# Optimization experiments

Hardware: AMD Instinct MI355X
Metric: run time of the kernel (lower is better)

The kernel has to match this reference:

```python
import jax, jax.numpy as jnp
import numpy as np

MAX_REL = 7  # maxRelativeDist

def _rel_pos_table(L, max_rel):
    # |i-j|, with distances beyond max_rel mapped to max_rel + log2(d - max_rel), clipped to [0, 2*max_rel]
    idx = jnp.arange(L)
    d = jnp.abs(idx[:, None] - idx[None, :]).astype(jnp.float32)
    far = d > max_rel
    d = jnp.where(far, max_rel + jnp.log2(jnp.maximum(d - max_rel, 1.0)), d)
    return jnp.clip(d, 0, 2 * max_rel).astype(jnp.int32)  # [L, L]

def setup_inputs() -> dict:
    key = jax.random.key(0)
    ks = jax.random.split(key, 16)
    B, L, C, P, H, DK = 8, 2048, 512, 64, 8, 64
    s = 0.02
    inp = {
        'qx': jax.random.normal(ks[0], (B, L, C), jnp.float32),
        'kx': jax.random.normal(ks[1], (B, L, C), jnp.float32),
        'vx': jax.random.normal(ks[2], (B, L, C), jnp.float32),
        'maskPAD': jnp.ones((B, L, L), jnp.int32),
        # pseudoAttn: Linear(C, P)
        'Wp': jax.random.normal(ks[3], (C, P), jnp.float32) * s,
        'bp': jnp.zeros((P,), jnp.float32),
        # WQ/WK: Linear(C, dkEnhance*DK*H) with dkEnhance=1
        'Wq': jax.random.normal(ks[4], (C, H * DK), jnp.float32) * s,
        'bq': jnp.zeros((H * DK,), jnp.float32),
        'Wk': jax.random.normal(ks[5], (C, H * DK), jnp.float32) * s,
        'bk': jnp.zeros((H * DK,), jnp.float32),
        'Wv': jax.random.normal(ks[6], (C, H * DK), jnp.float32) * s,
        'bv': jnp.zeros((H * DK,), jnp.float32),
        'Wo': jax.random.normal(ks[7], (H * DK, C), jnp.float32) * s,
        'bo': jnp.zeros((C,), jnp.float32),
        # relative position embeddings: [2*MAX_REL+1, H]
        'embK': jax.random.normal(ks[8], (2 * MAX_REL + 1, H), jnp.float32) * s,
        'embB': jax.random.normal(ks[9], (2 * MAX_REL + 1, H), jnp.float32) * s,
    }
    return inp

def reference(qx, kx, vx, maskPAD, Wp, bp, Wq, bq, Wk, bk, Wv, bv, Wo, bo, embK, embB):
    # dropout is identity (eval mode); preScores=None
    B, L, C = qx.shape
    H = embK.shape[1]
    DK = Wv.shape[1] // H
    P = Wp.shape[1]

    # pseudo-token compression
    pScore = vx @ Wp + bp                                   # [B, L, P]
    mask = (maskPAD[:, 0] == 0)[:, :, None]                 # [B, L, 1]
    pScore = jnp.where(mask, jnp.float32(-2.0 ** 15), pScore)
    pAlpha = jax.nn.softmax(pScore, axis=1)                 # softmax over L
    kxc = jnp.einsum('blp,blc->bpc', pAlpha, kx)            # [B, P, C]
    vxc = jnp.einsum('blp,blc->bpc', pAlpha, vx)            # [B, P, C]
    pAlpha_d = jax.lax.stop_gradient(pAlpha)

    # multi-head projections
    q = (qx @ Wq + bq).reshape(B, L, H, DK)                 # [B, L, H, DK]
    k = (kxc @ Wk + bk).reshape(B, P, H, DK)
    v = (vxc @ Wv + bv).reshape(B, P, H, DK)

    scores = jnp.einsum('blhd,bphd->bhlp', q, k) / np.sqrt(DK)  # [B, H, L, P]

    # relative-position modulation
    relTab = _rel_pos_table(L, MAX_REL)                     # [L, L] int
    Kmat = jnp.transpose(embK[relTab], (2, 1, 0))           # [H, L, L]
    Bmat = jnp.transpose(embB[relTab], (2, 1, 0))           # [H, L, L]
    Kterm = jnp.einsum('hlm,bmp->bhlp', Kmat, pAlpha_d)
    Bterm = jnp.einsum('hlm,bmp->bhlp', Bmat, pAlpha_d)
    scores = scores * Kterm + Bterm

    alpha = jax.nn.softmax(scores, axis=3)                  # over pseudo tokens
    z = jnp.einsum('bhlp,bphd->blhd', alpha, v).reshape(B, L, H * DK)
    z = z @ Wo + bo                                         # [B, L, C]
    return z, pScore, scores
```

## Files before the change

kernel.cpp:

```cpp
#include <hip/hip_runtime.h>


typedef __attribute__((ext_vector_type(8))) short bhalf8;
typedef __attribute__((ext_vector_type(4))) float fx4;

__device__ __forceinline__ unsigned short f2bf(float f) {
  union { float f; unsigned u; } v; v.f = f;
  unsigned u = v.u + 0x7fffu + ((v.u >> 16) & 1u);
  return (unsigned short)(u >> 16);
}
__device__ __forceinline__ float bf2f(unsigned short h) {
  union { unsigned u; float f; } v; v.u = ((unsigned)h) << 16;
  return v.f;
}
__device__ __forceinline__ void gld16(const void* g, void* l) {
  __builtin_amdgcn_global_load_lds(
      (const __attribute__((address_space(1))) void*)g,
      (__attribute__((address_space(3))) void*)l, 16, 0, 0);
}

template <int BM, int BN, int CMODE, int AF32, int KSPLIT>
__global__ __launch_bounds__(256)
void gemm_mfma(const void* __restrict__ Av, const unsigned short* __restrict__ BT,
               const float* __restrict__ bias, void* __restrict__ Cout,
               int K, int lda, int ldbt, int ldc, int HDIV,
               long sAb, long sAh, long sBb, long sBh, long sCb, long sCh, long sCk,
               const int* __restrict__ mpad, float* __restrict__ aux)
{
  constexpr int NA = BM / 16, NB = BN / 16, NT = NA + NB;
  constexpr int WM = BM / 2, WN = BN / 2, FM = WM / 16, FN = WN / 16;
  __shared__ __align__(16) unsigned short lds[NT * 512];
  const int t = threadIdx.x, l = t & 63, w = t >> 6;
  const int wr = w >> 1, wc = w & 1;
  const int zz = blockIdx.z, b = zz / HDIV, h = zz % HDIV;
  const int row0 = KSPLIT ? 0 : blockIdx.y * BM;
  const int koff = KSPLIT ? blockIdx.y * K : 0;
  const long cko = KSPLIT ? (long)blockIdx.y * sCk : 0;
  const int col0 = blockIdx.x * BN;
  const unsigned short* Ag = (const unsigned short*)Av + b * sAb + h * sAh + (long)row0 * lda + koff;
  const float* AgF = (const float*)Av + b * sAb + h * sAh + (long)row0 * lda + koff;
  const unsigned short* Bg = BT + b * sBb + h * sBh + (long)col0 * ldbt + koff;
  const int lr = l & 15, lc = l >> 4;

  fx4 acc[FM][FN];
#pragma unroll
  for (int i = 0; i < FM; ++i)
#pragma unroll
    for (int j = 0; j < FN; ++j) acc[i][j] = fx4{0.f, 0.f, 0.f, 0.f};

  for (int k0 = 0; k0 < K; k0 += 32) {
#pragma unroll
    for (int i = 0; i < NT / 4; ++i) {
      const int tile = w + i * 4;
      if constexpr (AF32 == 1) {
        if (tile < NA) {
          const float* gf = AgF + (long)(tile * 16 + lr) * lda + k0 + lc * 8;
          float4 x = *(const float4*)gf, y = *(const float4*)(gf + 4);
          bhalf8 pk;
          pk[0] = (short)f2bf(x.x); pk[1] = (short)f2bf(x.y);
          pk[2] = (short)f2bf(x.z); pk[3] = (short)f2bf(x.w);
          pk[4] = (short)f2bf(y.x); pk[5] = (short)f2bf(y.y);
          pk[6] = (short)f2bf(y.z); pk[7] = (short)f2bf(y.w);
          *(bhalf8*)&lds[tile * 512 + l * 8] = pk;
        } else {
          gld16(Bg + (long)((tile - NA) * 16 + lr) * ldbt + k0 + lc * 8, &lds[tile * 512]);
        }
      } else if constexpr (AF32 == 2) {
        if (tile < NA) {
          const float* gf = (const float*)Av + (long)zz * sAb + (long)blockIdx.y * 131072
                            + (long)(tile * 16 + lr) * 512 + k0 + lc * 8;
          float4 x = make_float4(0.f, 0.f, 0.f, 0.f), y = x;
#pragma unroll
          for (int c = 0; c < 4; ++c) {
            float4 a = *(const float4*)(gf + (long)c * 32768);
            float4 bq = *(const float4*)(gf + (long)c * 32768 + 4);
            x.x += a.x; x.y += a.y; x.z += a.z; x.w += a.w;
            y.x += bq.x; y.y += bq.y; y.z += bq.z; y.w += bq.w;
          }
          bhalf8 pk;
          pk[0] = (short)f2bf(x.x); pk[1] = (short)f2bf(x.y);
          pk[2] = (short)f2bf(x.z); pk[3] = (short)f2bf(x.w);
          pk[4] = (short)f2bf(y.x); pk[5] = (short)f2bf(y.y);
          pk[6] = (short)f2bf(y.z); pk[7] = (short)f2bf(y.w);
          *(bhalf8*)&lds[tile * 512 + l * 8] = pk;
        } else {
          gld16(Bg + (long)((tile - NA) * 16 + lr) * ldbt + k0 + lc * 8, &lds[tile * 512]);
        }
      } else {
        const unsigned short* g = (tile < NA)
            ? Ag + (long)(tile * 16 + lr) * lda + k0 + lc * 8
            : Bg + (long)((tile - NA) * 16 + lr) * ldbt + k0 + lc * 8;
        gld16(g, &lds[tile * 512]);
      }
    }
    __syncthreads();
    bhalf8 af[FM], bf[FN];
#pragma unroll
    for (int i = 0; i < FM; ++i) af[i] = *(const bhalf8*)&lds[(wr * FM + i) * 512 + l * 8];
#pragma unroll
    for (int j = 0; j < FN; ++j) bf[j] = *(const bhalf8*)&lds[(NA + wc * FN + j) * 512 + l * 8];
#pragma unroll
    for (int i = 0; i < FM; ++i)
#pragma unroll
      for (int j = 0; j < FN; ++j)
        acc[i][j] = __builtin_amdgcn_mfma_f32_16x16x32_bf16(af[i], bf[j], acc[i][j], 0, 0, 0);
    __syncthreads();
  }

  if constexpr (CMODE == 3) {
    __shared__ float tbuf[64][65];
#pragma unroll
    for (int fm = 0; fm < FM; ++fm) {
#pragma unroll
      for (int fn = 0; fn < FN; ++fn) {
        const int rg0 = row0 + wr * WM + fm * 16 + lc * 4;
        const int cg = col0 + wc * WN + fn * 16 + lr;
        const float bb = bias[cg];
#pragma unroll
        for (int jj = 0; jj < 4; ++jj) {
          const int rg = rg0 + jj;
          float vv = acc[fm][fn][jj] + bb;
          if (mpad[((long)(rg >> 11)) * (2048L * 2048) + (rg & 2047)] == 0) vv = -32768.f;
          __builtin_nontemporal_store(vv, (float*)Cout + (long)rg * ldc + cg);
          tbuf[rg - row0][cg] = vv;
        }
      }
    }
    __syncthreads();
    const int b0 = row0 >> 11, l0b = row0 & 2047;
    const int pp = t >> 2, li0 = (t & 3) * 16;
    float* dst = aux + ((long)b0 * 64 + pp) * 2048 + l0b + li0;
#pragma unroll
    for (int i = 0; i < 16; i += 4) {
      float4 o = make_float4(tbuf[li0 + i][pp],     tbuf[li0 + i + 1][pp],
                             tbuf[li0 + i + 2][pp], tbuf[li0 + i + 3][pp]);
      *(float4*)(dst + i) = o;
    }
  } else {
#pragma unroll
    for (int fm = 0; fm < FM; ++fm) {
#pragma unroll
      for (int fn = 0; fn < FN; ++fn) {
        const int rg0 = row0 + wr * WM + fm * 16 + lc * 4;
        const int cg = col0 + wc * WN + fn * 16 + lr;
        float bb = 0.f;
        if constexpr (CMODE == 4) {
          bb = (zz == 0) ? bias[cg] : ((const float*)mpad)[cg];
        } else {
          bb = bias ? bias[cg] : 0.f;
        }
#pragma unroll
        for (int jj = 0; jj < 4; ++jj) {
          const int rg = rg0 + jj;
          const float v = acc[fm][fn][jj] + bb;
          if constexpr (CMODE == 0) {
            ((float*)Cout)[b * sCb + h * sCh + cko + (long)rg * ldc + cg] = v;
          } else if constexpr (CMODE == 1) {
            ((unsigned short*)Cout)[b * sCb + h * sCh + (long)rg * ldc + cg] = f2bf(v);
          } else if constexpr (CMODE == 2) {
            ((unsigned short*)Cout)[(((long)(rg >> 6) * 8 + (cg >> 6)) * 64 + (cg & 63)) * 64 + (rg & 63)] = f2bf(v);
          } else if constexpr (CMODE == 4) {
            if (zz == 0)
              ((unsigned short*)Cout)[(long)rg * ldc + cg] = f2bf(v);
            else
              ((unsigned short*)Cout)[262144 + (((long)(rg >> 6) * 8 + (cg >> 6)) * 64 + (cg & 63)) * 64 + (rg & 63)] = f2bf(v);
          } else {
            __builtin_nontemporal_store(v, (float*)Cout + b * sCb + h * sCh + cko + (long)rg * ldc + cg);
          }
        }
      }
    }
  }
}

__device__ __forceinline__ void tr_body(float (*tile)[65], const float* __restrict__ in,
                                        unsigned short* __restrict__ out,
                                        int R, int Cd, int r0, int c0, int t)
{
  const int tr = t >> 4, tc4 = (t & 15) * 4;
#pragma unroll
  for (int pass = 0; pass < 4; ++pass) {
    int r = pass * 16 + tr;
    float4 v = *(const float4*)(in + (long)(r0 + r) * Cd + c0 + tc4);
    tile[r][tc4] = v.x; tile[r][tc4 + 1] = v.y; tile[r][tc4 + 2] = v.z; tile[r][tc4 + 3] = v.w;
  }
  __syncthreads();
#pragma unroll
  for (int pass = 0; pass < 4; ++pass) {
    int c = pass * 16 + tr;
    ushort4 o;
    o.x = f2bf(tile[tc4][c]);     o.y = f2bf(tile[tc4 + 1][c]);
    o.z = f2bf(tile[tc4 + 2][c]); o.w = f2bf(tile[tc4 + 3][c]);
    *(ushort4*)(out + (long)(c0 + c) * R + r0 + tc4) = o;
  }
}

__global__ __launch_bounds__(256)
void tconv_prep(const float* Wq, const float* Wk, const float* Wv, const float* Wo, const float* Wp,
                const float* kx, const float* vx,
                unsigned short* WqT, unsigned short* WkT, unsigned short* WvT,
                unsigned short* WoT, unsigned short* WpT,
                unsigned short* kxT, unsigned short* vxT)
{
  __shared__ float tile[64][65];
  const int z = blockIdx.z;
  const long LC = 2048L * 512;
  const float* in; unsigned short* out; int R, Cd;
  if (z < 5) {
    if (blockIdx.y >= 8) return;
    R = 512;
    switch (z) {
      case 0: in = Wq; out = WqT; Cd = 512; break;
      case 1: in = Wk; out = WkT; Cd = 512; break;
      case 2: in = Wv; out = WvT; Cd = 512; break;
      case 3: in = Wo; out = WoT; Cd = 512; break;
      default: in = Wp; out = WpT; Cd = 64; break;
    }
    if ((int)blockIdx.x * 64 >= Cd) return;
  } else {
    const int zz = z - 5;
    in = (zz < 8) ? kx + zz * LC : vx + (zz - 8) * LC;
    out = (zz < 8) ? kxT + zz * LC : vxT + (zz - 8) * LC;
    R = 2048; Cd = 512;
  }
  tr_body(tile, in, out, R, Cd, blockIdx.y * 64, blockIdx.x * 64, threadIdx.x);
}

__global__ __launch_bounds__(256)
void softmax_scan(const float* __restrict__ pScoreT,
                  unsigned short* __restrict__ PSb, unsigned short* __restrict__ pA_bf)
{
  __shared__ float red[256];
  const int p = blockIdx.x, b = blockIdx.y, t = threadIdx.x;
  const float* row = pScoreT + ((size_t)b * 64 + p) * 2048;
  float4 va = ((const float4*)row)[t * 2], vb = ((const float4*)row)[t * 2 + 1];
  float v[8] = {va.x, va.y, va.z, va.w, vb.x, vb.y, vb.z, vb.w};
  float mx = v[0];
#pragma unroll
  for (int i = 1; i < 8; ++i) mx = fmaxf(mx, v[i]);
  red[t] = mx; __syncthreads();
  for (int s = 128; s > 0; s >>= 1) { if (t < s) red[t] = fmaxf(red[t], red[t + s]); __syncthreads(); }
  float m = red[0]; __syncthreads();
  float e[8]; float s = 0.f;
#pragma unroll
  for (int i = 0; i < 8; ++i) { e[i] = expf(v[i] - m); s += e[i]; }
  red[t] = s; __syncthreads();
  for (int o = 1; o < 256; o <<= 1) {
    float x = (t >= o) ? red[t - o] : 0.f;
    __syncthreads(); red[t] += x; __syncthreads();
  }
  float inv = 1.0f / red[255];
  float run = red[t] - s;
  size_t base = ((size_t)b * 64 + p) * 2048 + (size_t)t * 8;
#pragma unroll
  for (int i = 0; i < 8; ++i) {
    run += e[i];
    PSb[base + i] = f2bf(run * inv);
    pA_bf[base + i] = f2bf(e[i] * inv);
  }
}

__global__ __launch_bounds__(256)
void kb_make2(const unsigned short* __restrict__ PSb,
              const float* __restrict__ embK, const float* __restrict__ embB,
              ushort2* __restrict__ KB)
{
  const int L = 2048, STR = 338;
  __shared__ unsigned short psw[64 * STR];
  __shared__ float eKs[16][8], eBs[16][8];
  const int t = threadIdx.x, b = blockIdx.y, l0 = blockIdx.x * 64;
  if (t < 128) {
    int r = t >> 3, h = t & 7;
    eKs[r][h] = (r < 15) ? embK[r * 8 + h] : 0.f;
    eBs[r][h] = (r < 15) ? embB[r * 8 + h] : 0.f;
  }
  const int W0 = l0 - 136;
  const int w = t >> 6, ln = t & 63;
  for (int pr = w * 16; pr < w * 16 + 16; ++pr) {
    const unsigned short* src = PSb + ((long)b * 64 + pr) * 2048;
#pragma unroll
    for (int pass = 0; pass < 6; ++pass) {
      int j = pass * 64 + ln;
      if (j < 337) {
        int g = (j == 336) ? (L - 1) : (W0 + j);
        g = g < 0 ? 0 : (g > L - 1 ? L - 1 : g);
        psw[pr * STR + j] = src[g];
      }
    }
  }
  __syncthreads();
  const int p = ln;
  const int Btab[14] = {0,1,2,3,4,5,6,8,10,14,22,38,70,134};
  for (int step = 0; step < 16; ++step) {
    const int l = l0 + w * 16 + step;
    float U[15];
#pragma unroll
    for (int r = 0; r < 14; ++r) {
      int hi = l + Btab[r]; hi = hi > L - 1 ? L - 1 : hi;
      float u = bf2f(psw[p * STR + (hi - W0)]);
      const int lo = l - 1 - Btab[r];
      if (lo >= 0) u -= bf2f(psw[p * STR + (lo - W0)]);
      U[r] = u;
    }
    U[14] = bf2f(psw[p * STR + 336]);
    for (int h = 0; h < 8; ++h) {
      float Kt = 0.f, Bt = 0.f;
#pragma unroll
      for (int r = 0; r < 15; ++r) {
        Kt = fmaf(eKs[r][h] - eKs[r + 1][h], U[r], Kt);
        Bt = fmaf(eBs[r][h] - eBs[r + 1][h], U[r], Bt);
      }
      ushort2 o; o.x = f2bf(Kt); o.y = f2bf(Bt);
      KB[(((long)(b * 8 + h)) * L + l) * 64 + p] = o;
    }
  }
}

__global__ __launch_bounds__(256)
void attn_fused(const unsigned short* __restrict__ qb,
                const unsigned short* __restrict__ kp,
                const unsigned short* __restrict__ vpT,
                const ushort2* __restrict__ KB,
                float* __restrict__ sc_out,
                unsigned short* __restrict__ zpre)
{
  const int L = 2048;
  __shared__ __align__(16) unsigned short stg[24 * 512];
  unsigned short* qkb = &stg[8 * 512];
  const int t = threadIdx.x, l = t & 63, w = t >> 6, lr = l & 15, lc = l >> 4;
  const int flat = blockIdx.y * 16 + blockIdx.x;
  const int swz = (flat & 7) * 128 + (flat >> 3);
  const int z = swz >> 4, b = z >> 3, h = z & 7;
  const int l0 = (swz & 15) * 128;
  const unsigned short* Ag = qb + ((long)(b * L + l0)) * 512 + h * 64;
  const unsigned short* Bg = kp + (long)b * 64 * 512 + h * 64;
#pragma unroll
  for (int i = 0; i < 6; ++i) {
    const int tile = w + i * 4;
    const unsigned short* g;
    if (tile < 16) { int rt = tile >> 1, ks = tile & 1; g = Ag + (long)(rt * 16 + lr) * 512 + ks * 32 + lc * 8; }
    else { int j = tile - 16; int rt = j >> 1, ks = j & 1; g = Bg + (long)(rt * 16 + lr) * 512 + ks * 32 + lc * 8; }
    gld16(g, &stg[tile * 512]);
  }
  __syncthreads();
  const int wr = w >> 1, wc = w & 1;
  fx4 acc[4][2];
#pragma unroll
  for (int i = 0; i < 4; ++i)
#pragma unroll
    for (int j = 0; j < 2; ++j) acc[i][j] = fx4{0.f, 0.f, 0.f, 0.f};
#pragma unroll
  for (int ks = 0; ks < 2; ++ks) {
    bhalf8 af[4], bf[2];
#pragma unroll
    for (int i = 0; i < 4; ++i) af[i] = *(const bhalf8*)&stg[((wr * 4 + i) * 2 + ks) * 512 + l * 8];
#pragma unroll
    for (int j = 0; j < 2; ++j) bf[j] = *(const bhalf8*)&stg[(16 + (wc * 2 + j) * 2 + ks) * 512 + l * 8];
#pragma unroll
    for (int i = 0; i < 4; ++i)
#pragma unroll
      for (int j = 0; j < 2; ++j)
        acc[i][j] = __builtin_amdgcn_mfma_f32_16x16x32_bf16(af[i], bf[j], acc[i][j], 0, 0, 0);
  }
  __syncthreads();
#pragma unroll
  for (int fm = 0; fm < 4; ++fm)
#pragma unroll
    for (int fn = 0; fn < 2; ++fn)
#pragma unroll
      for (int jj = 0; jj < 4; ++jj) {
        const int row = wr * 64 + fm * 16 + lc * 4 + jj;
        const int col = wc * 32 + fn * 16 + lr;
        *(unsigned short*)((char*)qkb + ((row * 128 + col * 2) ^ ((row & 7) << 4))) = f2bf(acc[fm][fn][jj]);
      }
  __syncthreads();
  {
    const unsigned short* Vg = vpT + ((long)(b * 8 + h)) * 64 * 64;
#pragma unroll
    for (int i = 0; i < 2; ++i) {
      const int tile = w + i * 4, rt = tile >> 1, ks = tile & 1;
      gld16(Vg + (long)(rt * 16 + lr) * 64 + ks * 32 + lc * 8, &stg[tile * 512]);
    }
  }
  const int p = l;
  const ushort2* kbb = KB + (((long)(b * 8 + h)) * L + l0) * 64 + p;
  float* scb = sc_out + ((long)(b * 8 + h) * L + l0) * 64 + p;
  for (int c = 0; c < 8; ++c) {
    const int rbase = w * 32 + c * 4;
    float sv[4];
#pragma unroll
    for (int il = 0; il < 4; ++il) {
      const int row = rbase + il;
      const ushort2 kb = kbb[(long)row * 64];
      const float qkv = bf2f(*(const unsigned short*)((const char*)qkb + ((row * 128 + p * 2) ^ ((row & 7) << 4))));
      sv[il] = qkv * 0.125f * bf2f(kb.x) + bf2f(kb.y);
      __builtin_nontemporal_store(sv[il], scb + (long)row * 64);
    }
    float mx[4] = {sv[0], sv[1], sv[2], sv[3]};
#pragma unroll
    for (int o = 32; o > 0; o >>= 1)
#pragma unroll
      for (int il = 0; il < 4; ++il) mx[il] = fmaxf(mx[il], __shfl_xor(mx[il], o, 64));
    float ex[4], sm[4];
#pragma unroll
    for (int il = 0; il < 4; ++il) { ex[il] = __expf(sv[il] - mx[il]); sm[il] = ex[il]; }
#pragma unroll
    for (int o = 32; o > 0; o >>= 1)
#pragma unroll
      for (int il = 0; il < 4; ++il) sm[il] += __shfl_xor(sm[il], o, 64);
#pragma unroll
    for (int il = 0; il < 4; ++il) {
      const int row = rbase + il;
      *(unsigned short*)((char*)qkb + ((row * 128 + p * 2) ^ ((row & 7) << 4))) = f2bf(ex[il] / sm[il]);
    }
  }
  __syncthreads();
  fx4 a2[4][2];
#pragma unroll
  for (int i = 0; i < 4; ++i)
#pragma unroll
    for (int j = 0; j < 2; ++j) a2[i][j] = fx4{0.f, 0.f, 0.f, 0.f};
#pragma unroll
  for (int ks = 0; ks < 2; ++ks) {
    bhalf8 paf[4], pvf[2];
#pragma unroll
    for (int i = 0; i < 4; ++i) {
      const int row = (wr * 4 + i) * 16 + lr;
      paf[i] = *(const bhalf8*)((const char*)qkb + ((row * 128 + ks * 64 + lc * 16) ^ ((row & 7) << 4)));
    }
#pragma unroll
    for (int j = 0; j < 2; ++j)
      pvf[j] = *(const bhalf8*)&stg[(((wc * 2 + j) * 2 + ks) * 512) + l * 8];
#pragma unroll
    for (int i = 0; i < 4; ++i)
#pragma unroll
      for (int j = 0; j < 2; ++j)
        a2[i][j] = __builtin_amdgcn_mfma_f32_16x16x32_bf16(paf[i], pvf[j], a2[i][j], 0, 0, 0);
  }
#pragma unroll
  for (int fm = 0; fm < 4; ++fm)
#pragma unroll
    for (int fn = 0; fn < 2; ++fn)
#pragma unroll
      for (int jj = 0; jj < 4; ++jj) {
        const int row = wr * 64 + fm * 16 + lc * 4 + jj;
        const int col = wc * 32 + fn * 16 + lr;
        zpre[((long)(b * L + l0 + row)) * 512 + h * 64 + col] = f2bf(a2[fm][fn][jj]);
      }
}

extern "C" void kernel_launch(void* const* d_in, const int* in_sizes, int n_in,
                              void* d_out, int out_size, void* d_ws, size_t ws_size,
                              hipStream_t stream)
{
  const int B = 8, L = 2048, C = 512, P = 64;
  const float* qx = (const float*)d_in[0];
  const float* kx = (const float*)d_in[1];
  const float* vx = (const float*)d_in[2];
  const int* maskPAD = (const int*)d_in[3];
  const float* Wp = (const float*)d_in[4];
  const float* bp = (const float*)d_in[5];
  const float* Wq = (const float*)d_in[6];
  const float* bq = (const float*)d_in[7];
  const float* Wk = (const float*)d_in[8];
  const float* bk = (const float*)d_in[9];
  const float* Wv = (const float*)d_in[10];
  const float* bv = (const float*)d_in[11];
  const float* Wo = (const float*)d_in[12];
  const float* bo = (const float*)d_in[13];
  const float* embK = (const float*)d_in[14];
  const float* embB = (const float*)d_in[15];

  float* z_out  = (float*)d_out;
  float* ps_out = z_out + (size_t)B * L * C;
  float* sc_out = ps_out + (size_t)B * L * P;

  char* w8 = (char*)d_ws;
  size_t o = 0;
  auto take = [&](size_t n) { char* r = w8 + o; o += n; return r; };
  unsigned short* R_A  = (unsigned short*)take(16777216);
  unsigned short* R_B  = (unsigned short*)take(16777216);
  unsigned short* kxT  = (unsigned short*)take(16777216);
  unsigned short* vxT  = (unsigned short*)take(16777216);
  unsigned short* WqT  = (unsigned short*)take(524288);
  unsigned short* WkT  = (unsigned short*)take(524288);
  unsigned short* WvT  = (unsigned short*)take(524288);
  unsigned short* WoT  = (unsigned short*)take(524288);
  unsigned short* WpT  = (unsigned short*)take(65536);
  float* pScoreT       = (float*)take(4194304);
  unsigned short* PSb  = (unsigned short*)take(2097152);
  unsigned short* pAbf = (unsigned short*)take(2097152);
  float* pbuf          = (float*)take(8388608);
  unsigned short* kp   = (unsigned short*)take(1048576);
  unsigned short* vpT  = kp + 262144;
  ushort2* KB          = (ushort2*)take(33554432);

  tconv_prep<<<dim3(8, 32, 21), 256, 0, stream>>>(
      Wq, Wk, Wv, Wo, Wp, kx, vx, WqT, WkT, WvT, WoT, WpT, kxT, vxT);
  gemm_mfma<64, 64, 3, 1, 0><<<dim3(1, 256, 1), 256, 0, stream>>>(
      vx, WpT, bp, ps_out, 512, 512, 512, 64, 1, 0, 0, 0, 0, 0, 0, 0, maskPAD, pScoreT);
  softmax_scan<<<dim3(P, B), 256, 0, stream>>>(pScoreT, PSb, pAbf);
  kb_make2<<<dim3(L / 64, B), 256, 0, stream>>>(PSb, embK, embB, KB);
  gemm_mfma<64, 128, 0, 0, 1><<<dim3(4, 4, 16), 256, 0, stream>>>(
      pAbf, kxT, nullptr, pbuf, 512, 2048, 2048, 512, 2,
      131072, 0, 1048576, 8388608, 131072, 1048576, 32768, nullptr, nullptr);
  gemm_mfma<64, 128, 4, 2, 0><<<dim3(4, 8, 2), 256, 0, stream>>>(
      pbuf, WkT, bk, kp, 512, 512, 512, 512, 1,
      1048576, 0, 262144, 0, 0, 0, 0, (const int*)bv, nullptr);
  gemm_mfma<128, 128, 1, 1, 0><<<dim3(4, 128, 1), 256, 0, stream>>>(
      qx, WqT, bq, R_B, 512, 512, 512, 512, 1, 0, 0, 0, 0, 0, 0, 0, nullptr, nullptr);
  attn_fused<<<dim3(16, 64), 256, 0, stream>>>(
      R_B, kp, vpT, KB, sc_out, R_A);
  gemm_mfma<128, 128, 5, 0, 0><<<dim3(4, 128, 1), 256, 0, stream>>>(
      R_A, WoT, bo, z_out, 512, 512, 512, 512, 1, 0, 0, 0, 0, 0, 0, 0, nullptr, nullptr);
}
```

Before: 221.4 us.

## Merge independent small kernels into combined launches and prefetch KB into registers

Measured after the change: 201.5 us. 9.0% less time.

```diff
diff --git a/kernel.cpp b/kernel.cpp
--- a/kernel.cpp
+++ b/kernel.cpp
@@ -20,23 +20,24 @@
 }
 
 template <int BM, int BN, int CMODE, int AF32, int KSPLIT>
-__global__ __launch_bounds__(256)
-void gemm_mfma(const void* __restrict__ Av, const unsigned short* __restrict__ BT,
-               const float* __restrict__ bias, void* __restrict__ Cout,
-               int K, int lda, int ldbt, int ldc, int HDIV,
-               long sAb, long sAh, long sBb, long sBh, long sCb, long sCh, long sCk,
-               const int* __restrict__ mpad, float* __restrict__ aux)
+__device__ __forceinline__ void gemm_body(
+    int bxx, int byy, int bzz, char* smemc,
+    const void* __restrict__ Av, const unsigned short* __restrict__ BT,
+    const float* __restrict__ bias, void* __restrict__ Cout,
+    int K, int lda, int ldbt, int ldc, int HDIV,
+    long sAb, long sAh, long sBb, long sBh, long sCb, long sCh, long sCk,
+    const int* __restrict__ mpad, float* __restrict__ aux)
 {
   constexpr int NA = BM / 16, NB = BN / 16, NT = NA + NB;
   constexpr int WM = BM / 2, WN = BN / 2, FM = WM / 16, FN = WN / 16;
-  __shared__ __align__(16) unsigned short lds[NT * 512];
+  unsigned short* lds = (unsigned short*)smemc;
   const int t = threadIdx.x, l = t & 63, w = t >> 6;
   const int wr = w >> 1, wc = w & 1;
-  const int zz = blockIdx.z, b = zz / HDIV, h = zz % HDIV;
-  const int row0 = KSPLIT ? 0 : blockIdx.y * BM;
-  const int koff = KSPLIT ? blockIdx.y * K : 0;
-  const long cko = KSPLIT ? (long)blockIdx.y * sCk : 0;
-  const int col0 = blockIdx.x * BN;
+  const int zz = bzz, b = zz / HDIV, h = zz % HDIV;
+  const int row0 = KSPLIT ? 0 : byy * BM;
+  const int koff = KSPLIT ? byy * K : 0;
+  const long cko = KSPLIT ? (long)byy * sCk : 0;
+  const int col0 = bxx * BN;
   const unsigned short* Ag = (const unsigned short*)Av + b * sAb + h * sAh + (long)row0 * lda + koff;
   const float* AgF = (const float*)Av + b * sAb + h * sAh + (long)row0 * lda + koff;
   const unsigned short* Bg = BT + b * sBb + h * sBh + (long)col0 * ldbt + koff;
@@ -67,7 +68,7 @@
         }
       } else if constexpr (AF32 == 2) {
         if (tile < NA) {
-          const float* gf = (const float*)Av + (long)zz * sAb + (long)blockIdx.y * 131072
+          const float* gf = (const float*)Av + (long)zz * sAb + (long)byy * 131072
                             + (long)(tile * 16 + lr) * 512 + k0 + lc * 8;
           float4 x = make_float4(0.f, 0.f, 0.f, 0.f), y = x;
 #pragma unroll
@@ -108,7 +109,7 @@
   }
 
   if constexpr (CMODE == 3) {
-    __shared__ float tbuf[64][65];
+    float (*tbuf)[65] = (float(*)[65])(smemc + NT * 1024);
 #pragma unroll
     for (int fm = 0; fm < FM; ++fm) {
 #pragma unroll
@@ -173,6 +174,118 @@
   }
 }
 
+template <int BM, int BN, int CMODE, int AF32, int KSPLIT>
+__global__ __launch_bounds__(256)
+void gemm_mfma(const void* __restrict__ Av, const unsigned short* __restrict__ BT,
+               const float* __restrict__ bias, void* __restrict__ Cout,
+               int K, int lda, int ldbt, int ldc, int HDIV,
+               long sAb, long sAh, long sBb, long sBh, long sCb, long sCh, long sCk,
+               const int* __restrict__ mpad, float* __restrict__ aux)
+{
+  constexpr int SM = (BM / 16 + BN / 16) * 1024 + (CMODE == 3 ? 16640 : 0);
+  __shared__ __align__(16) char smem[SM];
+  gemm_body<BM, BN, CMODE, AF32, KSPLIT>(blockIdx.x, blockIdx.y, blockIdx.z, smem,
+      Av, BT, bias, Cout, K, lda, ldbt, ldc, HDIV,
+      sAb, sAh, sBb, sBh, sCb, sCh, sCk, mpad, aux);
+}
+
+__device__ __forceinline__ void kb_body(int bx, int by, char* smemc,
+    const unsigned short* __restrict__ PSb,
+    const float* __restrict__ embK, const float* __restrict__ embB,
+    ushort2* __restrict__ KB)
+{
+  const int L = 2048, STR = 338;
+  unsigned short* psw = (unsigned short*)smemc;
+  float (*eKs)[8] = (float(*)[8])(smemc + 43264);
+  float (*eBs)[8] = (float(*)[8])(smemc + 43264 + 512);
+  const int t = threadIdx.x, b = by, l0 = bx * 64;
+  if (t < 128) {
+    int r = t >> 3, h = t & 7;
+    eKs[r][h] = (r < 15) ? embK[r * 8 + h] : 0.f;
+    eBs[r][h] = (r < 15) ? embB[r * 8 + h] : 0.f;
+  }
+  const int W0 = l0 - 136;
+  const int w = t >> 6, ln = t & 63;
+  for (int pr = w * 16; pr < w * 16 + 16; ++pr) {
+    const unsigned short* src = PSb + ((long)b * 64 + pr) * 2048;
+#pragma unroll
+    for (int pass = 0; pass < 6; ++pass) {
+      int j = pass * 64 + ln;
+      if (j < 337) {
+        int g = (j == 336) ? (L - 1) : (W0 + j);
+        g = g < 0 ? 0 : (g > L - 1 ? L - 1 : g);
+        psw[pr * STR + j] = src[g];
+      }
+    }
+  }
+  __syncthreads();
+  const int p = ln;
+  const int Btab[14] = {0,1,2,3,4,5,6,8,10,14,22,38,70,134};
+  for (int step = 0; step < 16; ++step) {
+    const int l = l0 + w * 16 + step;
+    float U[15];
+#pragma unroll
+    for (int r = 0; r < 14; ++r) {
+      int hi = l + Btab[r]; hi = hi > L - 1 ? L - 1 : hi;
+      float u = bf2f(psw[p * STR + (hi - W0)]);
+      const int lo = l - 1 - Btab[r];
+      if (lo >= 0) u -= bf2f(psw[p * STR + (lo - W0)]);
+      U[r] = u;
+    }
+    U[14] = bf2f(psw[p * STR + 336]);
+    for (int h = 0; h < 8; ++h) {
+      float Kt = 0.f, Bt = 0.f;
+#pragma unroll
+      for (int r = 0; r < 15; ++r) {
+        Kt = fmaf(eKs[r][h] - eKs[r + 1][h], U[r], Kt);
+        Bt = fmaf(eBs[r][h] - eBs[r + 1][h], U[r], Bt);
+      }
+      ushort2 o; o.x = f2bf(Kt); o.y = f2bf(Bt);
+      KB[(((long)(b * 8 + h)) * L + l) * 64 + p] = o;
+    }
+  }
+}
+
+__global__ __launch_bounds__(256)
+void combo1(const unsigned short* __restrict__ pAbf, const unsigned short* __restrict__ kxT,
+            float* __restrict__ pbuf,
+            const unsigned short* __restrict__ PSb,
+            const float* __restrict__ embK, const float* __restrict__ embB,
+            ushort2* __restrict__ KB)
+{
+  __shared__ __align__(16) char smem[44544];
+  const int id = blockIdx.x;
+  if (id < 256) {
+    gemm_body<64, 128, 0, 0, 1>(id & 3, (id >> 2) & 3, id >> 4, smem,
+        pAbf, kxT, nullptr, pbuf, 512, 2048, 2048, 512, 2,
+        131072, 0, 1048576, 8388608, 131072, 1048576, 32768, nullptr, nullptr);
+  } else {
+    const int r = id - 256;
+    kb_body(r & 31, r >> 5, smem, PSb, embK, embB, KB);
+  }
+}
+
+__global__ __launch_bounds__(256)
+void combo2(const float* __restrict__ pbuf, const unsigned short* __restrict__ WkT,
+            const float* __restrict__ bk, const float* __restrict__ bv,
+            unsigned short* __restrict__ kp,
+            const float* __restrict__ qx, const unsigned short* __restrict__ WqT,
+            const float* __restrict__ bq, unsigned short* __restrict__ qbf)
+{
+  __shared__ __align__(16) char smem[16384];
+  const int id = blockIdx.x;
+  if (id < 64) {
+    gemm_body<64, 128, 4, 2, 0>(id & 3, (id >> 2) & 7, id >> 5, smem,
+        pbuf, WkT, bk, kp, 512, 512, 512, 512, 1,
+        1048576, 0, 262144, 0, 0, 0, 0, (const int*)bv, nullptr);
+  } else {
+    const int r = id - 64;
+    gemm_body<128, 128, 1, 1, 0>(r & 3, r >> 2, 0, smem,
+        qx, WqT, bq, qbf, 512, 512, 512, 512, 1,
+        0, 0, 0, 0, 0, 0, 0, nullptr, nullptr);
+  }
+}
+
 __device__ __forceinline__ void tr_body(float (*tile)[65], const float* __restrict__ in,
                                         unsigned short* __restrict__ out,
                                         int R, int Cd, int r0, int c0, int t)
@@ -261,62 +374,6 @@
 }
 
 __global__ __launch_bounds__(256)
-void kb_make2(const unsigned short* __restrict__ PSb,
-              const float* __restrict__ embK, const float* __restrict__ embB,
-              ushort2* __restrict__ KB)
-{
-  const int L = 2048, STR = 338;
-  __shared__ unsigned short psw[64 * STR];
-  __shared__ float eKs[16][8], eBs[16][8];
-  const int t = threadIdx.x, b = blockIdx.y, l0 = blockIdx.x * 64;
-  if (t < 128) {
-    int r = t >> 3, h = t & 7;
-    eKs[r][h] = (r < 15) ? embK[r * 8 + h] : 0.f;
-    eBs[r][h] = (r < 15) ? embB[r * 8 + h] : 0.f;
-  }
-  const int W0 = l0 - 136;
-  const int w = t >> 6, ln = t & 63;
-  for (int pr = w * 16; pr < w * 16 + 16; ++pr) {
-    const unsigned short* src = PSb + ((long)b * 64 + pr) * 2048;
-#pragma unroll
-    for (int pass = 0; pass < 6; ++pass) {
-      int j = pass * 64 + ln;
-      if (j < 337) {
-        int g = (j == 336) ? (L - 1) : (W0 + j);
-        g = g < 0 ? 0 : (g > L - 1 ? L - 1 : g);
-        psw[pr * STR + j] = src[g];
-      }
-    }
-  }
-  __syncthreads();
-  const int p = ln;
-  const int Btab[14] = {0,1,2,3,4,5,6,8,10,14,22,38,70,134};
-  for (int step = 0; step < 16; ++step) {
-    const int l = l0 + w * 16 + step;
-    float U[15];
-#pragma unroll
-    for (int r = 0; r < 14; ++r) {
-      int hi = l + Btab[r]; hi = hi > L - 1 ? L - 1 : hi;
-      float u = bf2f(psw[p * STR + (hi - W0)]);
-      const int lo = l - 1 - Btab[r];
-      if (lo >= 0) u -= bf2f(psw[p * STR + (lo - W0)]);
-      U[r] = u;
-    }
-    U[14] = bf2f(psw[p * STR + 336]);
-    for (int h = 0; h < 8; ++h) {
-      float Kt = 0.f, Bt = 0.f;
-#pragma unroll
-      for (int r = 0; r < 15; ++r) {
-        Kt = fmaf(eKs[r][h] - eKs[r + 1][h], U[r], Kt);
-        Bt = fmaf(eBs[r][h] - eBs[r + 1][h], U[r], Bt);
-      }
-      ushort2 o; o.x = f2bf(Kt); o.y = f2bf(Bt);
-      KB[(((long)(b * 8 + h)) * L + l) * 64 + p] = o;
-    }
-  }
-}
-
-__global__ __launch_bounds__(256)
 void attn_fused(const unsigned short* __restrict__ qb,
                 const unsigned short* __restrict__ kp,
                 const unsigned short* __restrict__ vpT,
@@ -342,6 +399,11 @@
     else { int j = tile - 16; int rt = j >> 1, ks = j & 1; g = Bg + (long)(rt * 16 + lr) * 512 + ks * 32 + lc * 8; }
     gld16(g, &stg[tile * 512]);
   }
+  const ushort2* kbb = KB + (((long)(b * 8 + h)) * L + l0) * 64 + l;
+  unsigned int kbreg[32];
+#pragma unroll
+  for (int i = 0; i < 32; ++i)
+    kbreg[i] = *(const unsigned int*)(kbb + ((long)(w * 32 + i)) * 64);
   __syncthreads();
   const int wr = w >> 1, wc = w & 1;
   fx4 acc[4][2];
@@ -383,17 +445,17 @@
     }
   }
   const int p = l;
-  const ushort2* kbb = KB + (((long)(b * 8 + h)) * L + l0) * 64 + p;
   float* scb = sc_out + ((long)(b * 8 + h) * L + l0) * 64 + p;
+#pragma unroll
   for (int c = 0; c < 8; ++c) {
     const int rbase = w * 32 + c * 4;
     float sv[4];
 #pragma unroll
     for (int il = 0; il < 4; ++il) {
       const int row = rbase + il;
-      const ushort2 kb = kbb[(long)row * 64];
+      const unsigned int kbw = kbreg[c * 4 + il];
       const float qkv = bf2f(*(const unsigned short*)((const char*)qkb + ((row * 128 + p * 2) ^ ((row & 7) << 4))));
-      sv[il] = qkv * 0.125f * bf2f(kb.x) + bf2f(kb.y);
+      sv[il] = qkv * 0.125f * bf2f((unsigned short)(kbw & 0xffffu)) + bf2f((unsigned short)(kbw >> 16));
       __builtin_nontemporal_store(sv[il], scb + (long)row * 64);
     }
     float mx[4] = {sv[0], sv[1], sv[2], sv[3]};
@@ -492,7 +554,6 @@
   unsigned short* pAbf = (unsigned short*)take(2097152);
   float* pbuf          = (float*)take(8388608);
   unsigned short* kp   = (unsigned short*)take(1048576);
-  unsigned short* vpT  = kp + 262144;
   ushort2* KB          = (ushort2*)take(33554432);
 
   tconv_prep<<<dim3(8, 32, 21), 256, 0, stream>>>(
@@ -500,17 +561,10 @@
   gemm_mfma<64, 64, 3, 1, 0><<<dim3(1, 256, 1), 256, 0, stream>>>(
       vx, WpT, bp, ps_out, 512, 512, 512, 64, 1, 0, 0, 0, 0, 0, 0, 0, maskPAD, pScoreT);
   softmax_scan<<<dim3(P, B), 256, 0, stream>>>(pScoreT, PSb, pAbf);
-  kb_make2<<<dim3(L / 64, B), 256, 0, stream>>>(PSb, embK, embB, KB);
-  gemm_mfma<64, 128, 0, 0, 1><<<dim3(4, 4, 16), 256, 0, stream>>>(
-      pAbf, kxT, nullptr, pbuf, 512, 2048, 2048, 512, 2,
-      131072, 0, 1048576, 8388608, 131072, 1048576, 32768, nullptr, nullptr);
-  gemm_mfma<64, 128, 4, 2, 0><<<dim3(4, 8, 2), 256, 0, stream>>>(
-      pbuf, WkT, bk, kp, 512, 512, 512, 512, 1,
-      1048576, 0, 262144, 0, 0, 0, 0, (const int*)bv, nullptr);
-  gemm_mfma<128, 128, 1, 1, 0><<<dim3(4, 128, 1), 256, 0, stream>>>(
-      qx, WqT, bq, R_B, 512, 512, 512, 512, 1, 0, 0, 0, 0, 0, 0, 0, nullptr, nullptr);
+  combo1<<<dim3(512), 256, 0, stream>>>(pAbf, kxT, pbuf, PSb, embK, embB, KB);
+  combo2<<<dim3(576), 256, 0, stream>>>(pbuf, WkT, bk, bv, kp, qx, WqT, bq, R_B);
   attn_fused<<<dim3(16, 64), 256, 0, stream>>>(
-      R_B, kp, vpT, KB, sc_out, R_A);
+      R_B, kp, kp + 262144, KB, sc_out, R_A);
   gemm_mfma<128, 128, 5, 0, 0><<<dim3(4, 128, 1), 256, 0, stream>>>(
       R_A, WoT, bo, z_out, 512, 512, 512, 512, 1, 0, 0, 0, 0, 0, 0, 0, nullptr, nullptr);
 }
```
